# Kernel optimization log

Measured on AMD Instinct MI355X. Metric: run time of the kernel, lower is better.

## Reference

```python
import jax, jax.numpy as jnp
import numpy as np

DECAY = 0.8
EPS = 1e-5
H, C, D = 1, 4096, 512   # num_codebooks, codebook_size, dim
B, N = 8, 4096           # batch, tokens


def l2norm(t):
    return t / jnp.clip(jnp.linalg.norm(t, axis=-1, keepdims=True), 1e-12, None)


def setup_inputs() -> dict:
    key = jax.random.key(0)
    k1, k2, k3 = jax.random.split(key, 3)
    x = jax.random.normal(k1, (B, N, D), jnp.float32)
    embed = l2norm(jax.random.normal(k2, (H, C, D), jnp.float32))  # codebook rows are unit-norm
    cluster_size = jax.random.uniform(k3, (H, C), jnp.float32) * 10.0
    embed_avg = embed * cluster_size[..., None]
    return {"x": x, "embed": embed, "cluster_size": cluster_size, "embed_avg": embed_avg}


def reference(x, embed, cluster_size, embed_avg):
    # pack: 'h * d' with h = 1 codebook
    flatten = x.reshape(H, B * N, D)
    # cosine-sim distances (inputs assumed pre-l2norm'd by wrapper; embed is unit-norm)
    dist = jnp.einsum('hnd,hcd->hnc', flatten, embed)          # (h, n, c)
    # gumbel_sample with temperature 0 / eval == argmax
    embed_ind = jnp.argmax(dist, axis=-1)                      # (h, n)
    onehot = jax.nn.one_hot(embed_ind, C, dtype=flatten.dtype) # (h, n, c)
    # training-path quantize via one-hot matmul
    quantize = jnp.einsum('hnc,hcd->hnd', onehot, embed).reshape(B, N, D)
    # EMA codebook update
    bins = onehot.sum(axis=1)                                  # (h, c)
    new_cluster = cluster_size * DECAY + bins * (1.0 - DECAY)
    embed_sum = jnp.einsum('hnd,hnc->hcd', flatten, onehot)    # (h, c, d)
    new_embed_avg = embed_avg * DECAY + embed_sum * (1.0 - DECAY)
    tot = new_cluster.sum(axis=-1, keepdims=True)
    smoothed = (new_cluster + EPS) / (tot + C * EPS) * tot     # laplace_smoothing * total
    new_embed = l2norm(new_embed_avg / smoothed[..., None])
    return (quantize,
            embed_ind.reshape(B, N),
            dist.reshape(B, N, C),
            new_cluster,
            new_embed_avg,
            new_embed)
```

## Files before the change

kernel.cpp:

```cpp
#include <hip/hip_runtime.h>
#include <hip/hip_fp16.h>
#include <cstdint>
#include <cstddef>

#define CB    4096
#define DD    512
#define M_TOK 32768
#define DECAY_F 0.8f
#define OMD_F   0.2f
#define EPS_F   1e-5f

#define OFF_QUANT ((size_t)0)
#define SZ_QUANT  ((size_t)M_TOK * DD)
#define OFF_IND   (OFF_QUANT + SZ_QUANT)
#define SZ_IND    ((size_t)M_TOK)
#define OFF_DIST  (OFF_IND + SZ_IND)
#define SZ_DIST   ((size_t)M_TOK * CB)
#define OFF_NC    (OFF_DIST + SZ_DIST)
#define SZ_NC     ((size_t)CB)
#define OFF_AVG   (OFF_NC + SZ_NC)
#define SZ_AVG    ((size_t)CB * DD)
#define OFF_NEMB  (OFF_AVG + SZ_AVG)

typedef unsigned short ushort_b;
typedef __attribute__((ext_vector_type(8))) short f16x8;
typedef __attribute__((ext_vector_type(4))) float f32x4;

__global__ __launch_bounds__(256) void k_init(const float* __restrict__ eavg,
                                              float* __restrict__ avg_out,
                                              int* __restrict__ bins,
                                              float* __restrict__ tot) {
  size_t id = (size_t)blockIdx.x * 256 + threadIdx.x;
  float4 v = *(const float4*)(eavg + id * 4);
  float4 o;
  o.x = v.x * DECAY_F; o.y = v.y * DECAY_F; o.z = v.z * DECAY_F; o.w = v.w * DECAY_F;
  *(float4*)(avg_out + id * 4) = o;
  if (id < CB) bins[id] = 0;
  if (id == CB) *tot = 0.0f;
}

__global__ __launch_bounds__(256) void k_split(const float* __restrict__ src,
                                               ushort_b* __restrict__ hi,
                                               ushort_b* __restrict__ lo) {
  size_t id = (size_t)blockIdx.x * 256 + threadIdx.x;
  const float* p = src + id * 8;
  float4 v0 = *(const float4*)p;
  float4 v1 = *(const float4*)(p + 4);
  float f[8] = {v0.x, v0.y, v0.z, v0.w, v1.x, v1.y, v1.z, v1.w};
  ushort_b h[8], l[8];
#pragma unroll
  for (int j = 0; j < 8; ++j) {
    __half hh = __float2half(f[j]);
    h[j] = __half_as_ushort(hh);
    float r = f[j] - __half2float(hh);
    l[j] = __half_as_ushort(__float2half(r));
  }
  uint4 H, L;
  H.x = h[0] | ((unsigned)h[1] << 16); H.y = h[2] | ((unsigned)h[3] << 16);
  H.z = h[4] | ((unsigned)h[5] << 16); H.w = h[6] | ((unsigned)h[7] << 16);
  L.x = l[0] | ((unsigned)l[1] << 16); L.y = l[2] | ((unsigned)l[3] << 16);
  L.z = l[4] | ((unsigned)l[5] << 16); L.w = l[6] | ((unsigned)l[7] << 16);
  *(uint4*)(hi + id * 8) = H;
  *(uint4*)(lo + id * 8) = L;
}

#define TSZ 4096

__device__ __forceinline__ void gload16(const void* g, void* l) {
  __builtin_amdgcn_global_load_lds((const __attribute__((address_space(1))) unsigned int*)g,
                                   (__attribute__((address_space(3))) unsigned int*)l,
                                   16, 0, 0);
}

__global__ __launch_bounds__(256) void k_dist_mfma(const ushort_b* __restrict__ Xhi,
                                                   const ushort_b* __restrict__ Xlo,
                                                   const ushort_b* __restrict__ Ehi,
                                                   const ushort_b* __restrict__ Elo,
                                                   float* __restrict__ dist) {
  __shared__ __align__(16) ushort_b lds[4 * TSZ];
  const int tid  = threadIdx.x;
  const int lane = tid & 63;
  const int wid  = tid >> 6;
  const int wr   = wid >> 1;
  const int wc   = wid & 1;
  const int bn   = blockIdx.x;
  const int bm   = blockIdx.y;

  const size_t abase = (size_t)bm * 128 * DD;
  const size_t bbase = (size_t)bn * 128 * DD;

  const int chunk0 = tid;
  const int chunk1 = tid + 256;
  const int row0 = chunk0 >> 2, slot0 = chunk0 & 3;
  const int row1 = chunk1 >> 2, slot1 = chunk1 & 3;
  const int q0 = slot0 ^ ((row0 >> 1) & 3);
  const int q1 = slot1 ^ ((row1 >> 1) & 3);
  const size_t g0 = (size_t)row0 * DD + q0 * 8;
  const size_t g1 = (size_t)row1 * DD + q1 * 8;
  const int lb0 = (wid * 64) * 8;
  const int lb1 = (wid * 64 + 256) * 8;

  f32x4 acc[4][4];
#pragma unroll
  for (int i = 0; i < 4; ++i)
#pragma unroll
    for (int j = 0; j < 4; ++j) acc[i][j] = (f32x4){0.f, 0.f, 0.f, 0.f};

  const int qr = lane >> 4;
  int aoff[4], boff[4];
#pragma unroll
  for (int mi = 0; mi < 4; ++mi) {
    int row = wr * 64 + mi * 16 + (lane & 15);
    aoff[mi] = row * 32 + ((qr ^ ((row >> 1) & 3)) << 3);
  }
#pragma unroll
  for (int ni = 0; ni < 4; ++ni) {
    int col = wc * 64 + ni * 16 + (lane & 15);
    boff[ni] = col * 32 + ((qr ^ ((col >> 1) & 3)) << 3);
  }

  for (int kt = 0; kt < DD; kt += 32) {
    gload16(Xhi + abase + g0 + kt, &lds[0 * TSZ + lb0]);
    gload16(Xhi + abase + g1 + kt, &lds[0 * TSZ + lb1]);
    gload16(Xlo + abase + g0 + kt, &lds[1 * TSZ + lb0]);
    gload16(Xlo + abase + g1 + kt, &lds[1 * TSZ + lb1]);
    gload16(Ehi + bbase + g0 + kt, &lds[2 * TSZ + lb0]);
    gload16(Ehi + bbase + g1 + kt, &lds[2 * TSZ + lb1]);
    gload16(Elo + bbase + g0 + kt, &lds[3 * TSZ + lb0]);
    gload16(Elo + bbase + g1 + kt, &lds[3 * TSZ + lb1]);
    __syncthreads();

    f16x8 ah[4], al[4], bh[4], bl[4];
#pragma unroll
    for (int mi = 0; mi < 4; ++mi) {
      ah[mi] = *(const f16x8*)&lds[0 * TSZ + aoff[mi]];
      al[mi] = *(const f16x8*)&lds[1 * TSZ + aoff[mi]];
    }
#pragma unroll
    for (int ni = 0; ni < 4; ++ni) {
      bh[ni] = *(const f16x8*)&lds[2 * TSZ + boff[ni]];
      bl[ni] = *(const f16x8*)&lds[3 * TSZ + boff[ni]];
    }
#pragma unroll
    for (int mi = 0; mi < 4; ++mi)
#pragma unroll
      for (int ni = 0; ni < 4; ++ni) {
        acc[mi][ni] = __builtin_amdgcn_mfma_f32_16x16x32_f16(ah[mi], bh[ni], acc[mi][ni], 0, 0, 0);
        acc[mi][ni] = __builtin_amdgcn_mfma_f32_16x16x32_f16(al[mi], bh[ni], acc[mi][ni], 0, 0, 0);
        acc[mi][ni] = __builtin_amdgcn_mfma_f32_16x16x32_f16(ah[mi], bl[ni], acc[mi][ni], 0, 0, 0);
      }
    __syncthreads();
  }

  const int rbase = bm * 128 + wr * 64 + (lane >> 4) * 4;
  const int cbase = bn * 128 + wc * 64 + (lane & 15);
#pragma unroll
  for (int mi = 0; mi < 4; ++mi)
#pragma unroll
    for (int r = 0; r < 4; ++r) {
      float* drow = dist + (size_t)(rbase + mi * 16 + r) * CB + cbase;
#pragma unroll
      for (int ni = 0; ni < 4; ++ni) drow[ni * 16] = acc[mi][ni][r];
    }
}

__global__ __launch_bounds__(256) void k_argmax(const float* __restrict__ dist,
                                                float* __restrict__ ind_f,
                                                int* __restrict__ idx_ws,
                                                int* __restrict__ bins) {
  const int row = blockIdx.x;
  const float* p = dist + (size_t)row * CB;
  const int tid = threadIdx.x;
  float best = -3.402823466e38f;
  int bi = 0;
#pragma unroll
  for (int it = 0; it < 4; ++it) {
    int j4 = (tid + it * 256) << 2;
    float4 v = *(const float4*)(p + j4);
    if (v.x > best) { best = v.x; bi = j4; }
    if (v.y > best) { best = v.y; bi = j4 + 1; }
    if (v.z > best) { best = v.z; bi = j4 + 2; }
    if (v.w > best) { best = v.w; bi = j4 + 3; }
  }
  for (int off = 32; off; off >>= 1) {
    float ov = __shfl_down(best, off);
    int   oi = __shfl_down(bi, off);
    if (ov > best || (ov == best && oi < bi)) { best = ov; bi = oi; }
  }
  __shared__ float sv[4];
  __shared__ int   si[4];
  int wid = tid >> 6;
  if ((tid & 63) == 0) { sv[wid] = best; si[wid] = bi; }
  __syncthreads();
  if (tid == 0) {
#pragma unroll
    for (int w = 1; w < 4; ++w)
      if (sv[w] > best || (sv[w] == best && si[w] < bi)) { best = sv[w]; bi = si[w]; }
    ind_f[row]  = (float)bi;
    idx_ws[row] = bi;
    atomicAdd(&bins[bi], 1);
  }
}

__global__ __launch_bounds__(256) void k_quant_scatter(const float* __restrict__ X,
                                                       const float* __restrict__ E,
                                                       const int* __restrict__ idx_ws,
                                                       float* __restrict__ quant,
                                                       float* __restrict__ avg) {
  size_t id = (size_t)blockIdx.x * 256 + threadIdx.x;
  int n  = (int)(id >> 7);
  int d4 = (int)(id & 127) << 2;
  int c  = idx_ws[n];
  float4 e = *(const float4*)(E + (size_t)c * DD + d4);
  *(float4*)(quant + (size_t)n * DD + d4) = e;
  float4 xv = *(const float4*)(X + (size_t)n * DD + d4);
  float* dst = avg + (size_t)c * DD + d4;
  atomicAdd(dst + 0, OMD_F * xv.x);
  atomicAdd(dst + 1, OMD_F * xv.y);
  atomicAdd(dst + 2, OMD_F * xv.z);
  atomicAdd(dst + 3, OMD_F * xv.w);
}

__global__ __launch_bounds__(256) void k_cluster(const float* __restrict__ cs,
                                                 const int* __restrict__ bins,
                                                 float* __restrict__ nc_out,
                                                 float* __restrict__ tot) {
  int c = blockIdx.x * 256 + threadIdx.x;
  float nc = DECAY_F * cs[c] + OMD_F * (float)bins[c];
  nc_out[c] = nc;
  float s = nc;
  for (int off = 32; off; off >>= 1) s += __shfl_down(s, off);
  if ((threadIdx.x & 63) == 0) atomicAdd(tot, s);
}

__global__ __launch_bounds__(128) void k_norm(const float* __restrict__ avg,
                                              const float* __restrict__ nc,
                                              const float* __restrict__ tot,
                                              float* __restrict__ out) {
  int c = blockIdx.x;
  int tid = threadIdx.x;
  const float* row = avg + (size_t)c * DD;
  float4 v = *(const float4*)(row + tid * 4);
  float ss = v.x * v.x + v.y * v.y + v.z * v.z + v.w * v.w;
  for (int off = 32; off; off >>= 1) ss += __shfl_down(ss, off);
  __shared__ float s2[2];
  if ((tid & 63) == 0) s2[tid >> 6] = ss;
  __syncthreads();
  float sumsq = s2[0] + s2[1];
  float t = *tot;
  float sm = (nc[c] + EPS_F) / (t + (float)CB * EPS_F) * t;
  float nrm = sqrtf(sumsq) / sm;
  float denom = fmaxf(nrm, 1e-12f);
  float scale = 1.0f / (sm * denom);
  float4 o;
  o.x = v.x * scale; o.y = v.y * scale; o.z = v.z * scale; o.w = v.w * scale;
  *(float4*)(out + (size_t)c * DD + tid * 4) = o;
}

extern "C" void kernel_launch(void* const* d_in, const int* in_sizes, int n_in,
                              void* d_out, int out_size, void* d_ws, size_t ws_size,
                              hipStream_t stream) {
  const float* x     = (const float*)d_in[0];
  const float* embed = (const float*)d_in[1];
  const float* cs    = (const float*)d_in[2];
  const float* eavg  = (const float*)d_in[3];

  float* out    = (float*)d_out;
  float* quant  = out + OFF_QUANT;
  float* indf   = out + OFF_IND;
  float* dist   = out + OFF_DIST;
  float* ncout  = out + OFF_NC;
  float* avgout = out + OFF_AVG;
  float* nemb   = out + OFF_NEMB;

  int*   idx_ws = (int*)d_ws;
  int*   bins   = idx_ws + M_TOK;
  float* tot    = (float*)(bins + CB);

  ushort_b* xhi = (ushort_b*)quant;
  ushort_b* xlo = xhi + (size_t)M_TOK * DD;
  ushort_b* ehi = (ushort_b*)nemb;
  ushort_b* elo = ehi + (size_t)CB * DD;

  k_init<<<dim3(2048), dim3(256), 0, stream>>>(eavg, avgout, bins, tot);
  k_split<<<dim3(M_TOK * DD / 8 / 256), dim3(256), 0, stream>>>(x, xhi, xlo);
  k_split<<<dim3(CB * DD / 8 / 256), dim3(256), 0, stream>>>(embed, ehi, elo);
  k_dist_mfma<<<dim3(CB / 128, M_TOK / 128), dim3(256), 0, stream>>>(xhi, xlo, ehi, elo, dist);
  k_argmax<<<dim3(M_TOK), dim3(256), 0, stream>>>(dist, indf, idx_ws, bins);
  k_quant_scatter<<<dim3(16384), dim3(256), 0, stream>>>(x, embed, idx_ws, quant, avgout);
  k_cluster<<<dim3(16), dim3(256), 0, stream>>>(cs, bins, ncout, tot);
  k_norm<<<dim3(CB), dim3(128), 0, stream>>>(avgout, ncout, tot, nemb);
}
```

Baseline: 1.296 ms.

## Replace atomic embed-sum scatter with counting-sort bucketed per-code reduction

Instead of having every token atomically add its vector into the codebook average, tokens are bucketed by code with a prefix scan and a cursor scatter. One block per code then sums its tokens in registers and writes the quantized rows and the EMA update directly. This removes 16M float atomics and the separate decay-init pass, at the cost of three extra launches and a serial per-code loop that may be load-imbalanced.

```diff
diff --git a/kernel.cpp b/kernel.cpp
--- a/kernel.cpp
+++ b/kernel.cpp
@@ -26,17 +26,11 @@
 typedef __attribute__((ext_vector_type(8))) short f16x8;
 typedef __attribute__((ext_vector_type(4))) float f32x4;
 
-__global__ __launch_bounds__(256) void k_init(const float* __restrict__ eavg,
-                                              float* __restrict__ avg_out,
-                                              int* __restrict__ bins,
+__global__ __launch_bounds__(256) void k_init(int* __restrict__ bins,
                                               float* __restrict__ tot) {
-  size_t id = (size_t)blockIdx.x * 256 + threadIdx.x;
-  float4 v = *(const float4*)(eavg + id * 4);
-  float4 o;
-  o.x = v.x * DECAY_F; o.y = v.y * DECAY_F; o.z = v.z * DECAY_F; o.w = v.w * DECAY_F;
-  *(float4*)(avg_out + id * 4) = o;
+  int id = blockIdx.x * 256 + threadIdx.x;
   if (id < CB) bins[id] = 0;
-  if (id == CB) *tot = 0.0f;
+  if (id == 0) *tot = 0.0f;
 }
 
 __global__ __launch_bounds__(256) void k_split(const float* __restrict__ src,
@@ -202,23 +196,69 @@
   }
 }
 
-__global__ __launch_bounds__(256) void k_quant_scatter(const float* __restrict__ X,
-                                                       const float* __restrict__ E,
-                                                       const int* __restrict__ idx_ws,
-                                                       float* __restrict__ quant,
-                                                       float* __restrict__ avg) {
-  size_t id = (size_t)blockIdx.x * 256 + threadIdx.x;
-  int n  = (int)(id >> 7);
-  int d4 = (int)(id & 127) << 2;
-  int c  = idx_ws[n];
+__global__ __launch_bounds__(256) void k_scan(const int* __restrict__ bins,
+                                              int* __restrict__ cursor) {
+  const int tid  = threadIdx.x;
+  const int lane = tid & 63;
+  const int wid  = tid >> 6;
+  int v[16];
+  const int base = tid * 16;
+  int run = 0;
+#pragma unroll
+  for (int i = 0; i < 16; ++i) { int t = bins[base + i]; v[i] = run; run += t; }
+  int x = run;
+  for (int d = 1; d < 64; d <<= 1) {
+    int y = __shfl_up(x, d);
+    if (lane >= d) x += y;
+  }
+  __shared__ int wtot[4];
+  if (lane == 63) wtot[wid] = x;
+  __syncthreads();
+  int woff = 0;
+  for (int w = 0; w < wid; ++w) woff += wtot[w];
+  int ex = woff + x - run;
+#pragma unroll
+  for (int i = 0; i < 16; ++i) cursor[base + i] = ex + v[i];
+}
+
+__global__ __launch_bounds__(256) void k_scatter_ids(const int* __restrict__ idx_ws,
+                                                     int* __restrict__ cursor,
+                                                     int* __restrict__ tlist) {
+  int n = blockIdx.x * 256 + threadIdx.x;
+  int c = idx_ws[n];
+  int slot = atomicAdd(&cursor[c], 1);
+  tlist[slot] = n;
+}
+
+__global__ __launch_bounds__(128) void k_embed_sum(const float* __restrict__ X,
+                                                   const float* __restrict__ E,
+                                                   const float* __restrict__ eavg,
+                                                   const int* __restrict__ cursor,
+                                                   const int* __restrict__ bins,
+                                                   const int* __restrict__ tlist,
+                                                   float* __restrict__ quant,
+                                                   float* __restrict__ avg) {
+  const int c   = blockIdx.x;
+  const int tid = threadIdx.x;
+  const int d4  = tid * 4;
+  const int end = cursor[c];
+  const int cnt = bins[c];
+  const int start = end - cnt;
   float4 e = *(const float4*)(E + (size_t)c * DD + d4);
-  *(float4*)(quant + (size_t)n * DD + d4) = e;
-  float4 xv = *(const float4*)(X + (size_t)n * DD + d4);
-  float* dst = avg + (size_t)c * DD + d4;
-  atomicAdd(dst + 0, OMD_F * xv.x);
-  atomicAdd(dst + 1, OMD_F * xv.y);
-  atomicAdd(dst + 2, OMD_F * xv.z);
-  atomicAdd(dst + 3, OMD_F * xv.w);
+  float4 s = {0.f, 0.f, 0.f, 0.f};
+  for (int t = start; t < end; ++t) {
+    int n = tlist[t];
+    float4 xv = *(const float4*)(X + (size_t)n * DD + d4);
+    s.x += xv.x; s.y += xv.y; s.z += xv.z; s.w += xv.w;
+    *(float4*)(quant + (size_t)n * DD + d4) = e;
+  }
+  float4 ea = *(const float4*)(eavg + (size_t)c * DD + d4);
+  float4 o;
+  o.x = DECAY_F * ea.x + OMD_F * s.x;
+  o.y = DECAY_F * ea.y + OMD_F * s.y;
+  o.z = DECAY_F * ea.z + OMD_F * s.z;
+  o.w = DECAY_F * ea.w + OMD_F * s.w;
+  *(float4*)(avg + (size_t)c * DD + d4) = o;
 }
 
 __global__ __launch_bounds__(256) void k_cluster(const float* __restrict__ cs,
@@ -282,12 +322,17 @@
   ushort_b* ehi = (ushort_b*)nemb;
   ushort_b* elo = ehi + (size_t)CB * DD;
 
-  k_init<<<dim3(2048), dim3(256), 0, stream>>>(eavg, avgout, bins, tot);
+  int* tlist  = (int*)nemb;
+  int* cursor = tlist + M_TOK;
+
+  k_init<<<dim3(16), dim3(256), 0, stream>>>(bins, tot);
   k_split<<<dim3(M_TOK * DD / 8 / 256), dim3(256), 0, stream>>>(x, xhi, xlo);
   k_split<<<dim3(CB * DD / 8 / 256), dim3(256), 0, stream>>>(embed, ehi, elo);
   k_dist_mfma<<<dim3(CB / 128, M_TOK / 128), dim3(256), 0, stream>>>(xhi, xlo, ehi, elo, dist);
   k_argmax<<<dim3(M_TOK), dim3(256), 0, stream>>>(dist, indf, idx_ws, bins);
-  k_quant_scatter<<<dim3(16384), dim3(256), 0, stream>>>(x, embed, idx_ws, quant, avgout);
+  k_scan<<<dim3(1), dim3(256), 0, stream>>>(bins, cursor);
+  k_scatter_ids<<<dim3(M_TOK / 256), dim3(256), 0, stream>>>(idx_ws, cursor, tlist);
+  k_embed_sum<<<dim3(CB), dim3(128), 0, stream>>>(x, embed, eavg, cursor, bins, tlist, quant, avgout);
   k_cluster<<<dim3(16), dim3(256), 0, stream>>>(cs, bins, ncout, tot);
   k_norm<<<dim3(CB), dim3(128), 0, stream>>>(avgout, ncout, tot, nemb);
 }
```

Result: faster. 1.111 ms (-14.3%).
